# Kernel optimization log

Measured on AMD Instinct MI355X. Metric: run time of the kernel, lower is better.

The kernel has to match this reference:

```python
import jax, jax.numpy as jnp
import numpy as np

S, H, NH, DS = 4096, 1024, 2, 64   # seq_len, hidden, num_heads, static_in_size
HD = H // NH                        # head_dim = 512
EPS = 1e-5                          # eqx.nn.LayerNorm default eps


def setup_inputs() -> dict:
    key = jax.random.key(0)
    ks = jax.random.split(key, 11)
    sc = lambda n: 1.0 / np.sqrt(n)
    return {
        "inputs": jax.random.normal(ks[0], (S, H), jnp.float32),
        "static_data": jax.random.normal(ks[1], (DS,), jnp.float32),
        "base_mask": jax.random.randint(ks[2], (S,), 0, 2).astype(bool),
        "Wq": jax.random.normal(ks[3], (H, H), jnp.float32) * sc(H),
        "Wk": jax.random.normal(ks[4], (H, H), jnp.float32) * sc(H),
        "Wv": jax.random.normal(ks[5], (H, H), jnp.float32) * sc(H),
        "Wo": jax.random.normal(ks[6], (H, H), jnp.float32) * sc(H),
        "Ws": jax.random.normal(ks[7], (H, DS), jnp.float32) * sc(DS),
        "bs": jax.random.normal(ks[8], (H,), jnp.float32) * 0.01,
        "ln_w": jnp.ones((H,), jnp.float32),
        "ln_b": jnp.zeros((H,), jnp.float32),
    }


def reference(inputs, static_data, base_mask, Wq, Wk, Wv, Wo, Ws, bs, ln_w, ln_b):
    # static embedding injected into keys/values
    semb = Ws @ static_data + bs                      # [H]
    kv_in = inputs + semb[None, :]                    # [S, H]

    # per-head projections (eqx Linear: y = W @ x, no bias in MHA projections)
    q = (inputs @ Wq.T).reshape(S, NH, HD)
    k = (kv_in @ Wk.T).reshape(S, NH, HD)
    v = (kv_in @ Wv.T).reshape(S, NH, HD)

    logits = jnp.einsum('qhd,khd->hqk', q, k) / np.sqrt(HD)  # [NH, S, S]

    # head 0: irregular mask (base_mask broadcast over queries); head 1: all-ones
    irregular = jnp.broadcast_to(base_mask[None, :], (S, S))
    mask = jnp.stack([irregular, jnp.ones((S, S), bool)], axis=0)  # [2, S, S]
    logits = jnp.where(mask, logits, jnp.finfo(logits.dtype).min)

    attn = jax.nn.softmax(logits, axis=-1)
    ctx = jnp.einsum('hqk,khd->qhd', attn, v).reshape(S, H)
    out = ctx @ Wo.T                                  # output projection

    # dropout_rate = 0 -> identity; residual + per-token LayerNorm
    res = out + inputs
    mu = res.mean(-1, keepdims=True)
    var = res.var(-1, keepdims=True)
    return (res - mu) / jnp.sqrt(var + EPS) * ln_w + ln_b
```

## Files before the change

kernel.cpp:

```cpp
#include <hip/hip_runtime.h>
#include <stdint.h>

#define S_LEN  4096
#define HID    1024
#define NHEAD  2
#define HDIM   512
#define KS_STRIDE 520
#define LN_EPS 1e-5f
#define PADK   4224
#define CH1    832

typedef __bf16 bf16x8 __attribute__((ext_vector_type(8)));
typedef float  f32x4  __attribute__((ext_vector_type(4)));

__device__ __forceinline__ float b2f(unsigned short u) {
    return __uint_as_float(((unsigned int)u) << 16);
}
__device__ __forceinline__ unsigned short f2b(float f) {
    unsigned int u = __float_as_uint(f);
    u += 0x7FFFu + ((u >> 16) & 1u);
    return (unsigned short)(u >> 16);
}

__device__ __forceinline__ void async_cp16(const void* g, void* l) {
    __builtin_amdgcn_global_load_lds(
        (const __attribute__((address_space(1))) unsigned int*)g,
        (__attribute__((address_space(3))) unsigned int*)l, 16, 0, 0);
}

__global__ void k_cvt4s(const float* __restrict__ i0, const float* __restrict__ i1,
                        const float* __restrict__ i2, const float* __restrict__ i3,
                        unsigned short* __restrict__ o0, unsigned short* __restrict__ o1,
                        unsigned short* __restrict__ o2, unsigned short* __restrict__ o3,
                        const float* __restrict__ Ws, const float* __restrict__ sd,
                        const float* __restrict__ bs, float* __restrict__ semb,
                        const int* __restrict__ msk, int* __restrict__ cidx,
                        int* __restrict__ nactp) {
    int z = blockIdx.y;
    if (z == 4) {
        int j = blockIdx.x * blockDim.x + threadIdx.x;
        if (j >= HID) return;
        float acc = bs[j];
        const float* row = Ws + j * 64;
        #pragma unroll
        for (int d = 0; d < 64; ++d) acc += row[d] * sd[d];
        semb[j] = acc;
        return;
    }
    if (z == 5) {
        if (blockIdx.x != 0) return;
        __shared__ int cnts[256];
        __shared__ int bases[256];
        int t = threadIdx.x;
        int c = 0;
        #pragma unroll
        for (int i = 0; i < 16; ++i) c += (msk[t * 16 + i] != 0);
        cnts[t] = c;
        __syncthreads();
        if (t == 0) {
            int b = 0;
            for (int k = 0; k < 256; ++k) { bases[k] = b; b += cnts[k]; }
            nactp[0] = b;
        }
        __syncthreads();
        int b = bases[t];
        #pragma unroll
        for (int i = 0; i < 16; ++i)
            if (msk[t * 16 + i] != 0) cidx[b++] = t * 16 + i;
        return;
    }
    const float* in = z == 0 ? i0 : z == 1 ? i1 : z == 2 ? i2 : i3;
    unsigned short* o = z == 0 ? o0 : z == 1 ? o1 : z == 2 ? o2 : o3;
    int i = (blockIdx.x * blockDim.x + threadIdx.x) * 8;
    float4 a = *(const float4*)(in + i);
    float4 b = *(const float4*)(in + i + 4);
    unsigned short r[8] = {f2b(a.x), f2b(a.y), f2b(a.z), f2b(a.w),
                           f2b(b.x), f2b(b.y), f2b(b.z), f2b(b.w)};
    *(uint4*)(o + i) = *(const uint4*)r;
}

__global__ void k_kvin(const float* __restrict__ X,
                       const float* __restrict__ semb,
                       unsigned short* __restrict__ Xb,
                       unsigned short* __restrict__ kv) {
    int idx = (blockIdx.x * blockDim.x + threadIdx.x) * 8;
    if (idx >= S_LEN * HID) return;
    int col = idx & (HID - 1);
    float4 a = *(const float4*)(X + idx);
    float4 b = *(const float4*)(X + idx + 4);
    unsigned short xo[8] = {f2b(a.x), f2b(a.y), f2b(a.z), f2b(a.w),
                            f2b(b.x), f2b(b.y), f2b(b.z), f2b(b.w)};
    *(uint4*)(Xb + idx) = *(const uint4*)xo;
    unsigned short o[8];
    o[0] = f2b(a.x + semb[col + 0]);
    o[1] = f2b(a.y + semb[col + 1]);
    o[2] = f2b(a.z + semb[col + 2]);
    o[3] = f2b(a.w + semb[col + 3]);
    o[4] = f2b(b.x + semb[col + 4]);
    o[5] = f2b(b.y + semb[col + 5]);
    o[6] = f2b(b.z + semb[col + 6]);
    o[7] = f2b(b.w + semb[col + 7]);
    *(uint4*)(kv + idx) = *(const uint4*)o;
}

__device__ __forceinline__
void gemm128(const unsigned short* __restrict__ A,
             const unsigned short* __restrict__ B,
             unsigned short* __restrict__ Cb,
             int bx, int nx, int ldc) {
    __shared__ unsigned short As[2][128 * 32];
    __shared__ unsigned short Bs[2][128 * 32];
    int tid  = threadIdx.x;
    int wave = tid >> 6, lane = tid & 63;
    int quad = lane >> 4, l16 = lane & 15;
    int wm = wave >> 1, wn = wave & 1;
    int m0 = (bx / nx) * 128, n0 = (bx % nx) * 128;

    auto stage = [&](int k0, int b) {
        #pragma unroll
        for (int i = 0; i < 2; ++i) {
            int c = tid + i * 256;
            async_cp16(A + (m0 + (c >> 2)) * HID + k0 + (c & 3) * 8, As[b] + c * 8);
            async_cp16(B + (n0 + (c >> 2)) * HID + k0 + (c & 3) * 8, Bs[b] + c * 8);
        }
    };

    f32x4 zero = {0.f, 0.f, 0.f, 0.f};
    f32x4 acc[4][4];
    #pragma unroll
    for (int i = 0; i < 4; ++i)
        #pragma unroll
        for (int j = 0; j < 4; ++j) acc[i][j] = zero;

    stage(0, 0);
    for (int it = 0; it < HID / 32; ++it) {
        int b = it & 1;
        __syncthreads();
        if (it + 1 < HID / 32) stage((it + 1) * 32, b ^ 1);

        bf16x8 af[4], bfr[4];
        #pragma unroll
        for (int i = 0; i < 4; ++i)
            af[i] = *(const bf16x8*)(As[b] + (wm * 64 + i * 16 + l16) * 32 + quad * 8);
        #pragma unroll
        for (int j = 0; j < 4; ++j)
            bfr[j] = *(const bf16x8*)(Bs[b] + (wn * 64 + j * 16 + l16) * 32 + quad * 8);
        #pragma unroll
        for (int i = 0; i < 4; ++i)
            #pragma unroll
            for (int j = 0; j < 4; ++j)
                acc[i][j] = __builtin_amdgcn_mfma_f32_16x16x32_bf16(af[i], bfr[j], acc[i][j], 0, 0, 0);
    }

    #pragma unroll
    for (int i = 0; i < 4; ++i) {
        int rbase = m0 + wm * 64 + i * 16 + quad * 4;
        #pragma unroll
        for (int j = 0; j < 4; ++j) {
            int col = n0 + wn * 64 + j * 16 + l16;
            #pragma unroll
            for (int r = 0; r < 4; ++r)
                Cb[(size_t)(rbase + r) * ldc + col] = f2b(acc[i][j][r]);
        }
    }
}

__global__ __launch_bounds__(256)
void k_gemm_qkv(const unsigned short* __restrict__ Xb,
                const unsigned short* __restrict__ kvin,
                const unsigned short* __restrict__ Wqb,
                const unsigned short* __restrict__ Wkb,
                const unsigned short* __restrict__ Wvb,
                unsigned short* __restrict__ Qb,
                unsigned short* __restrict__ Kb,
                unsigned short* __restrict__ Vt) {
    int bx = (blockIdx.x & 7) * 32 + (blockIdx.x >> 3);
    int z = blockIdx.z;
    if (z == 0)      gemm128(Xb,   Wqb,  Qb,  bx,  8, HID);
    else if (z == 1) gemm128(kvin, Wkb,  Kb,  bx,  8, HID);
    else             gemm128(Wvb,  kvin, Vt,  bx, 32, S_LEN);
}

__global__ __launch_bounds__(256)
void k_gather(const unsigned short* __restrict__ Kb,
              const unsigned short* __restrict__ Vt,
              const int* __restrict__ cidx,
              const int* __restrict__ nactp,
              unsigned short* __restrict__ Kc,
              unsigned short* __restrict__ Vtc) {
    int nact = nactp[0];
    int gid = blockIdx.x * 256 + threadIdx.x;
    int idx = gid * 8;
    if (blockIdx.y == 0) {
        int j = idx >> 9, d = idx & 511;
        uint4 v = {0u, 0u, 0u, 0u};
        if (j < nact) v = *(const uint4*)(Kb + (size_t)cidx[j] * HID + d);
        *(uint4*)(Kc + (size_t)j * 512 + d) = v;
    } else {
        int d = idx / PADK, j0 = idx % PADK;
        unsigned short o[8];
        #pragma unroll
        for (int i = 0; i < 8; ++i) {
            int j = j0 + i;
            o[i] = (j < nact) ? Vt[(size_t)d * S_LEN + cidx[j]] : (unsigned short)0;
        }
        *(uint4*)(Vtc + (size_t)d * PADK + j0) = *(const uint4*)o;
    }
}

__global__ __launch_bounds__(256)
void k_gemm_o(const unsigned short* __restrict__ Opart,
              const float* __restrict__ Lbuf,
              const unsigned short* __restrict__ B,
              float* __restrict__ Cf,
              const float* __restrict__ Xres) {
    __shared__ unsigned short As[2][64 * 32];
    __shared__ unsigned short Bs[2][128 * 32];
    const size_t SH2 = (size_t)S_LEN * 512;
    int tid  = threadIdx.x;
    int wave = tid >> 6, lane = tid & 63;
    int quad = lane >> 4, l16 = lane & 15;
    int bx = (blockIdx.x & 7) * 64 + (blockIdx.x >> 3);
    int m0 = (bx >> 3) * 64, n0 = (bx & 7) * 128;

    int arow  = m0 + (tid >> 2);
    int acol8 = (tid & 3) * 8;
    float rinv[NHEAD];
    {
        float l0 = Lbuf[arow] + Lbuf[S_LEN + arow] + Lbuf[2 * S_LEN + arow];
        float l1 = 0.f;
        #pragma unroll
        for (int z = 3; z < 8; ++z) l1 += Lbuf[z * S_LEN + arow];
        rinv[0] = 1.f / l0;
        rinv[1] = 1.f / l1;
    }

    auto stageB = [&](int k0, int b) {
        #pragma unroll
        for (int i = 0; i < 2; ++i) {
            int c = tid + i * 256;
            async_cp16(B + (n0 + (c >> 2)) * HID + k0 + (c & 3) * 8, Bs[b] + c * 8);
        }
    };
    auto stageA = [&](int k0, int b) {
        int h = k0 >> 9;
        float rv = rinv[h];
        int lk = (k0 & 511) + acol8;
        const unsigned short* ap = Opart + (h ? 3 * SH2 : 0) + (size_t)arow * 512 + lk;
        float s[8] = {0.f, 0.f, 0.f, 0.f, 0.f, 0.f, 0.f, 0.f};
        int nz = h ? 5 : 3;
        for (int z = 0; z < nz; ++z) {
            uint4 v = *(const uint4*)(ap + (size_t)z * SH2);
            unsigned short us[8];
            *(uint4*)us = v;
            #pragma unroll
            for (int e = 0; e < 8; ++e) s[e] += b2f(us[e]);
        }
        unsigned short o8[8];
        #pragma unroll
        for (int e = 0; e < 8; ++e) o8[e] = f2b(s[e] * rv);
        *(uint4*)(As[b] + tid * 8) = *(const uint4*)o8;
    };

    f32x4 zero = {0.f, 0.f, 0.f, 0.f};
    f32x4 acc[4][2];
    #pragma unroll
    for (int i = 0; i < 4; ++i)
        #pragma unroll
        for (int j = 0; j < 2; ++j) acc[i][j] = zero;

    stageB(0, 0);
    stageA(0, 0);
    for (int it = 0; it < HID / 32; ++it) {
        int b = it & 1;
        __syncthreads();
        if (it + 1 < HID / 32) {
            stageB((it + 1) * 32, b ^ 1);
            stageA((it + 1) * 32, b ^ 1);
        }
        bf16x8 af[4], bfr[2];
        #pragma unroll
        for (int i = 0; i < 4; ++i)
            af[i] = *(const bf16x8*)(As[b] + (i * 16 + l16) * 32 + quad * 8);
        #pragma unroll
        for (int j = 0; j < 2; ++j)
            bfr[j] = *(const bf16x8*)(Bs[b] + (wave * 32 + j * 16 + l16) * 32 + quad * 8);
        #pragma unroll
        for (int i = 0; i < 4; ++i)
            #pragma unroll
            for (int j = 0; j < 2; ++j)
                acc[i][j] = __builtin_amdgcn_mfma_f32_16x16x32_bf16(af[i], bfr[j], acc[i][j], 0, 0, 0);
    }

    #pragma unroll
    for (int i = 0; i < 4; ++i) {
        int rbase = m0 + i * 16 + quad * 4;
        #pragma unroll
        for (int j = 0; j < 2; ++j) {
            int col = n0 + wave * 32 + j * 16 + l16;
            #pragma unroll
            for (int r = 0; r < 4; ++r) {
                size_t o = (size_t)(rbase + r) * HID + col;
                Cf[o] = acc[i][j][r] + Xres[o];
            }
        }
    }
}

__global__ __launch_bounds__(512, 2)
void k_flash(const unsigned short* __restrict__ Q,
             const unsigned short* __restrict__ Kb,
             const unsigned short* __restrict__ Vt,
             const unsigned short* __restrict__ Kc,
             const unsigned short* __restrict__ Vtc,
             const int* __restrict__ nactp,
             unsigned short* __restrict__ Opart,
             float* __restrict__ Lbuf) {
    __shared__ unsigned short Ks[2][32 * KS_STRIDE];
    __shared__ __bf16 Ps[2][128][40];
    int tid  = threadIdx.x;
    int wave = tid >> 6, lane = tid & 63;
    int quad = lane >> 4, l16 = lane & 15;
    int x = blockIdx.x, qtile = blockIdx.y;
    int head  = (x >= 3) ? 1 : 0;
    int split = head ? x - 3 : x;
    int nact  = nactp[0];

    int nit, base, krs, vrs;
    const unsigned short *Ksrc, *Vsrc;
    if (head == 0) {
        nit  = (nact + 95) / 96;
        base = split * nit * 32;
        Ksrc = Kc;  krs = 512;
        Vsrc = Vtc; vrs = PADK;
    } else {
        base = split * CH1;
        nit  = min(CH1 >> 5, (S_LEN - base) >> 5);
        Ksrc = Kb + HDIM;  krs = HID;
        Vsrc = Vt + (size_t)HDIM * S_LEN;
        vrs  = S_LEN;
    }

    int qrow = qtile * 128 + wave * 16 + l16;
    const unsigned short* qp = Q + qrow * HID + head * HDIM;
    bf16x8 qf[16];
    #pragma unroll
    for (int t = 0; t < 16; ++t) qf[t] = *(const bf16x8*)(qp + t * 32 + quad * 8);

    float lsum[4];
    #pragma unroll
    for (int r = 0; r < 4; ++r) lsum[r] = 0.f;
    f32x4 zero = {0.f, 0.f, 0.f, 0.f};
    f32x4 oacc[8][4];
    #pragma unroll
    for (int mt = 0; mt < 8; ++mt)
        #pragma unroll
        for (int nt = 0; nt < 4; ++nt) oacc[mt][nt] = zero;

    const float scale = 0.044194173824159216f;
    const unsigned short* vptr = Vsrc + (size_t)(wave * 64 + l16) * vrs + base + quad * 8;

    auto stageK = [&](int kt, int buf) {
        int kb = base + kt * 32;
        #pragma unroll
        for (int i = 0; i < 4; ++i) {
            int c = tid + i * 512;
            int row = c >> 6, col = (c & 63) * 8;
            async_cp16(Ksrc + (size_t)(kb + row) * krs + col, &Ks[buf][row * KS_STRIDE + col]);
        }
    };

    if (nit > 0) stageK(0, 0);

    bf16x8 vf[4];
    for (int it = 0; it < nit; ++it) {
        int cur = it & 1;
        __syncthreads();

        if (it + 1 < nit) stageK(it + 1, cur ^ 1);

        __builtin_amdgcn_s_setprio(1);
        if (it > 0) {
            #pragma unroll
            for (int mt = 0; mt < 8; ++mt) {
                bf16x8 pf = *(const bf16x8*)&Ps[cur ^ 1][mt * 16 + l16][quad * 8];
                #pragma unroll
                for (int nt = 0; nt < 4; ++nt)
                    oacc[mt][nt] = __builtin_amdgcn_mfma_f32_16x16x32_bf16(pf, vf[nt], oacc[mt][nt], 0, 0, 0);
            }
        }

        #pragma unroll
        for (int nt = 0; nt < 4; ++nt)
            vf[nt] = *(const bf16x8*)(vptr + (size_t)nt * 16 * vrs + it * 32);

        f32x4 sacc[2];
        sacc[0] = zero; sacc[1] = zero;
        #pragma unroll
        for (int nt = 0; nt < 2; ++nt)
            #pragma unroll
            for (int t = 0; t < 16; ++t) {
                bf16x8 kf = *(const bf16x8*)&Ks[cur][(nt * 16 + l16) * KS_STRIDE + t * 32 + quad * 8];
                sacc[nt] = __builtin_amdgcn_mfma_f32_16x16x32_bf16(qf[t], kf, sacc[nt], 0, 0, 0);
            }
        __builtin_amdgcn_s_setprio(0);

        bool keep0 = true, keep1 = true;
        if (head == 0) {
            int kb = base + it * 32;
            keep0 = kb + l16 < nact;
            keep1 = kb + 16 + l16 < nact;
        }
        #pragma unroll
        for (int r = 0; r < 4; ++r) {
            float p0 = keep0 ? __expf(fminf(sacc[0][r] * scale, 30.f)) : 0.f;
            float p1 = keep1 ? __expf(fminf(sacc[1][r] * scale, 30.f)) : 0.f;
            lsum[r] += p0 + p1;
            Ps[cur][wave * 16 + quad * 4 + r][l16]      = (__bf16)p0;
            Ps[cur][wave * 16 + quad * 4 + r][16 + l16] = (__bf16)p1;
        }
    }

    if (nit > 0) {
        int lastb = (nit - 1) & 1;
        __syncthreads();
        #pragma unroll
        for (int mt = 0; mt < 8; ++mt) {
            bf16x8 pf = *(const bf16x8*)&Ps[lastb][mt * 16 + l16][quad * 8];
            #pragma unroll
            for (int nt = 0; nt < 4; ++nt)
                oacc[mt][nt] = __builtin_amdgcn_mfma_f32_16x16x32_bf16(pf, vf[nt], oacc[mt][nt], 0, 0, 0);
        }
    }

    #pragma unroll
    for (int r = 0; r < 4; ++r) {
        float s = lsum[r];
        #pragma unroll
        for (int off = 1; off < 16; off <<= 1)
            s += __shfl_xor(s, off, 64);
        lsum[r] = s;
    }
    int slot = head ? 3 + split : split;
    int lrow = qtile * 128 + wave * 16 + quad * 4;
    if (l16 == 0) {
        #pragma unroll
        for (int r = 0; r < 4; ++r)
            Lbuf[slot * S_LEN + lrow + r] = lsum[r];
    }
    unsigned short* op = Opart + (size_t)slot * S_LEN * 512;
    #pragma unroll
    for (int mt = 0; mt < 8; ++mt)
        #pragma unroll
        for (int nt = 0; nt < 4; ++nt)
            #pragma unroll
            for (int r = 0; r < 4; ++r)
                op[(qtile * 128 + mt * 16 + quad * 4 + r) * 512 +
                   wave * 64 + nt * 16 + l16] = f2b(oacc[mt][nt][r]);
}

__global__ __launch_bounds__(256)
void k_ln(const float* __restrict__ res,
          const float* __restrict__ w,
          const float* __restrict__ b,
          float* __restrict__ out) {
    __shared__ float red[8];
    int s = blockIdx.x, tid = threadIdx.x;
    const float* row = res + s * HID;
    float x[4], s1 = 0.f, s2 = 0.f;
    #pragma unroll
    for (int i = 0; i < 4; ++i) {
        x[i] = row[tid + i * 256];
        s1 += x[i]; s2 += x[i] * x[i];
    }
    #pragma unroll
    for (int off = 1; off < 64; off <<= 1) {
        s1 += __shfl_xor(s1, off, 64);
        s2 += __shfl_xor(s2, off, 64);
    }
    int wave = tid >> 6;
    if ((tid & 63) == 0) { red[wave] = s1; red[4 + wave] = s2; }
    __syncthreads();
    s1 = red[0] + red[1] + red[2] + red[3];
    s2 = red[4] + red[5] + red[6] + red[7];
    float mu   = s1 * (1.f / HID);
    float var  = s2 * (1.f / HID) - mu * mu;
    float rstd = rsqrtf(var + LN_EPS);
    #pragma unroll
    for (int i = 0; i < 4; ++i) {
        int col = tid + i * 256;
        out[s * HID + col] = (x[i] - mu) * rstd * w[col] + b[col];
    }
}

extern "C" void kernel_launch(void* const* d_in, const int* in_sizes, int n_in,
                              void* d_out, int out_size, void* d_ws, size_t ws_size,
                              hipStream_t stream) {
    const float* X   = (const float*)d_in[0];
    const float* sd  = (const float*)d_in[1];
    const int*   msk = (const int*)d_in[2];
    const float* Wq  = (const float*)d_in[3];
    const float* Wk  = (const float*)d_in[4];
    const float* Wv  = (const float*)d_in[5];
    const float* Wo  = (const float*)d_in[6];
    const float* Wsp = (const float*)d_in[7];
    const float* bsp = (const float*)d_in[8];
    const float* lw  = (const float*)d_in[9];
    const float* lb  = (const float*)d_in[10];
    float* out = (float*)d_out;

    char* ws = (char*)d_ws;
    const size_t MB = 1ull << 20;
    float*          semb  = (float*)(ws);
    int*            cidx  = (int*)(ws + (16 << 10));
    int*            nactp = (int*)(ws + (48 << 10));
    float*          Lbuf  = (float*)(ws + (1ull << 16));
    unsigned short* Xb    = (unsigned short*)(ws + 1 * MB);
    unsigned short* kvin  = (unsigned short*)(ws + 9 * MB);
    unsigned short* Kc    = (unsigned short*)(ws + 1 * MB);
    unsigned short* Vtc   = (unsigned short*)(ws + 5 * MB + (256 << 10));
    unsigned short* Qb    = (unsigned short*)(ws + 17 * MB);
    unsigned short* Kb    = (unsigned short*)(ws + 25 * MB);
    unsigned short* Vt    = (unsigned short*)(ws + 33 * MB);
    unsigned short* Wqb   = (unsigned short*)(ws + 49 * MB);
    unsigned short* Wkb   = (unsigned short*)(ws + 51 * MB);
    unsigned short* Wvb   = (unsigned short*)(ws + 53 * MB);
    unsigned short* Wob   = (unsigned short*)(ws + 55 * MB);
    float*          resf  = (float*)(ws + 17 * MB);
    unsigned short* Opart = (unsigned short*)(ws + 57 * MB);

    const int SH = S_LEN * HID;
    const int WW = HID * HID;

    k_cvt4s<<<dim3(WW / 8 / 256, 6), dim3(256), 0, stream>>>(
        Wq, Wk, Wv, Wo, Wqb, Wkb, Wvb, Wob, Wsp, sd, bsp, semb, msk, cidx, nactp);

    k_kvin<<<dim3(SH / 8 / 256), dim3(256), 0, stream>>>(X, semb, Xb, kvin);

    k_gemm_qkv<<<dim3(256, 1, 3), dim3(256), 0, stream>>>(Xb, kvin, Wqb, Wkb, Wvb, Qb, Kb, Vt);

    k_gather<<<dim3(PADK * 512 / 8 / 256, 2), dim3(256), 0, stream>>>(
        Kb, Vt, cidx, nactp, Kc, Vtc);

    k_flash<<<dim3(8, S_LEN / 128), dim3(512), 0, stream>>>(
        Qb, Kb, Vt, Kc, Vtc, nactp, Opart, Lbuf);

    k_gemm_o<<<dim3(512), dim3(256), 0, stream>>>(Opart, Lbuf, Wob, resf, X);
    k_ln<<<dim3(S_LEN), dim3(256), 0, stream>>>(resf, lw, lb, out);
}
```

Before: 270.3 us.

## Fuse masked-key gather into the QKV projection GEMM via indexed row loads

Removes the separate gather kernel. The projection GEMM now computes head-0 K and V directly into compacted buffers, using the active-index list to choose which input rows it loads, and computes head-1 K/V into dedicated half-width buffers. Padded index entries are zero-filled so tiles past the active count read row 0 rather than garbage. This removes a kernel launch and the gather's read/write traffic, and skips projecting masked head-0 keys, but adds an indirect index load per staged row and a less uniform block dispatch.

```diff
diff --git a/kernel.cpp b/kernel.cpp
--- a/kernel.cpp
+++ b/kernel.cpp
@@ -51,6 +51,7 @@
         if (blockIdx.x != 0) return;
         __shared__ int cnts[256];
         __shared__ int bases[256];
+        __shared__ int nact_s;
         int t = threadIdx.x;
         int c = 0;
         #pragma unroll
@@ -61,12 +62,14 @@
             int b = 0;
             for (int k = 0; k < 256; ++k) { bases[k] = b; b += cnts[k]; }
             nactp[0] = b;
+            nact_s   = b;
         }
         __syncthreads();
         int b = bases[t];
         #pragma unroll
         for (int i = 0; i < 16; ++i)
             if (msk[t * 16 + i] != 0) cidx[b++] = t * 16 + i;
+        for (int j = nact_s + t; j < PADK; j += 256) cidx[j] = 0;
         return;
     }
     const float* in = z == 0 ? i0 : z == 1 ? i1 : z == 2 ? i2 : i3;
@@ -107,7 +110,8 @@
 void gemm128(const unsigned short* __restrict__ A,
              const unsigned short* __restrict__ B,
              unsigned short* __restrict__ Cb,
-             int bx, int nx, int ldc) {
+             int bx, int nx, int ldc,
+             const int* __restrict__ ra, const int* __restrict__ rb) {
     __shared__ unsigned short As[2][128 * 32];
     __shared__ unsigned short Bs[2][128 * 32];
     int tid  = threadIdx.x;
@@ -120,8 +124,12 @@
         #pragma unroll
         for (int i = 0; i < 2; ++i) {
             int c = tid + i * 256;
-            async_cp16(A + (m0 + (c >> 2)) * HID + k0 + (c & 3) * 8, As[b] + c * 8);
-            async_cp16(B + (n0 + (c >> 2)) * HID + k0 + (c & 3) * 8, Bs[b] + c * 8);
+            int arow = m0 + (c >> 2);
+            if (ra) arow = ra[arow];
+            int brow = n0 + (c >> 2);
+            if (rb) brow = rb[brow];
+            async_cp16(A + (size_t)arow * HID + k0 + (c & 3) * 8, As[b] + c * 8);
+            async_cp16(B + (size_t)brow * HID + k0 + (c & 3) * 8, Bs[b] + c * 8);
         }
     };
 
@@ -166,46 +174,24 @@
 }
 
 __global__ __launch_bounds__(256)
-void k_gemm_qkv(const unsigned short* __restrict__ Xb,
-                const unsigned short* __restrict__ kvin,
-                const unsigned short* __restrict__ Wqb,
-                const unsigned short* __restrict__ Wkb,
-                const unsigned short* __restrict__ Wvb,
-                unsigned short* __restrict__ Qb,
-                unsigned short* __restrict__ Kb,
-                unsigned short* __restrict__ Vt) {
-    int bx = (blockIdx.x & 7) * 32 + (blockIdx.x >> 3);
-    int z = blockIdx.z;
-    if (z == 0)      gemm128(Xb,   Wqb,  Qb,  bx,  8, HID);
-    else if (z == 1) gemm128(kvin, Wkb,  Kb,  bx,  8, HID);
-    else             gemm128(Wvb,  kvin, Vt,  bx, 32, S_LEN);
-}
-
-__global__ __launch_bounds__(256)
-void k_gather(const unsigned short* __restrict__ Kb,
-              const unsigned short* __restrict__ Vt,
-              const int* __restrict__ cidx,
-              const int* __restrict__ nactp,
-              unsigned short* __restrict__ Kc,
-              unsigned short* __restrict__ Vtc) {
-    int nact = nactp[0];
-    int gid = blockIdx.x * 256 + threadIdx.x;
-    int idx = gid * 8;
-    if (blockIdx.y == 0) {
-        int j = idx >> 9, d = idx & 511;
-        uint4 v = {0u, 0u, 0u, 0u};
-        if (j < nact) v = *(const uint4*)(Kb + (size_t)cidx[j] * HID + d);
-        *(uint4*)(Kc + (size_t)j * 512 + d) = v;
-    } else {
-        int d = idx / PADK, j0 = idx % PADK;
-        unsigned short o[8];
-        #pragma unroll
-        for (int i = 0; i < 8; ++i) {
-            int j = j0 + i;
-            o[i] = (j < nact) ? Vt[(size_t)d * S_LEN + cidx[j]] : (unsigned short)0;
-        }
-        *(uint4*)(Vtc + (size_t)d * PADK + j0) = *(const uint4*)o;
-    }
+void k_gemms(const unsigned short* __restrict__ Xb,
+             const unsigned short* __restrict__ kvin,
+             const unsigned short* __restrict__ Wqb,
+             const unsigned short* __restrict__ Wkb,
+             const unsigned short* __restrict__ Wvb,
+             const int* __restrict__ cidx,
+             unsigned short* __restrict__ Qb,
+             unsigned short* __restrict__ Kb1,
+             unsigned short* __restrict__ Vt1,
+             unsigned short* __restrict__ Kc,
+             unsigned short* __restrict__ Vtc) {
+    int g = blockIdx.x;
+    int b = (g & 7) * 97 + (g >> 3);
+    if (b < 256)      gemm128(Xb,   Wqb,             Qb,  b,        8, HID,   nullptr, nullptr);
+    else if (b < 384) gemm128(kvin, Wkb + 512 * HID, Kb1, b - 256,  4, 512,   nullptr, nullptr);
+    else if (b < 512) gemm128(Wvb + 512 * HID, kvin, Vt1, b - 384, 32, S_LEN, nullptr, nullptr);
+    else if (b < 644) gemm128(kvin, Wkb,             Kc,  b - 512,  4, 512,   cidx,    nullptr);
+    else              gemm128(Wvb,  kvin,            Vtc, b - 644, 33, PADK,  nullptr, cidx);
 }
 
 __global__ __launch_bounds__(256)
@@ -309,8 +295,8 @@
 
 __global__ __launch_bounds__(512, 2)
 void k_flash(const unsigned short* __restrict__ Q,
-             const unsigned short* __restrict__ Kb,
-             const unsigned short* __restrict__ Vt,
+             const unsigned short* __restrict__ Kb1,
+             const unsigned short* __restrict__ Vt1,
              const unsigned short* __restrict__ Kc,
              const unsigned short* __restrict__ Vtc,
              const int* __restrict__ nactp,
@@ -326,19 +312,16 @@
     int split = head ? x - 3 : x;
     int nact  = nactp[0];
 
-    int nit, base, krs, vrs;
+    int nit, base, vrs;
     const unsigned short *Ksrc, *Vsrc;
     if (head == 0) {
         nit  = (nact + 95) / 96;
         base = split * nit * 32;
-        Ksrc = Kc;  krs = 512;
-        Vsrc = Vtc; vrs = PADK;
+        Ksrc = Kc;  Vsrc = Vtc; vrs = PADK;
     } else {
         base = split * CH1;
         nit  = min(CH1 >> 5, (S_LEN - base) >> 5);
-        Ksrc = Kb + HDIM;  krs = HID;
-        Vsrc = Vt + (size_t)HDIM * S_LEN;
-        vrs  = S_LEN;
+        Ksrc = Kb1; Vsrc = Vt1; vrs = S_LEN;
     }
 
     int qrow = qtile * 128 + wave * 16 + l16;
@@ -366,7 +349,7 @@
         for (int i = 0; i < 4; ++i) {
             int c = tid + i * 512;
             int row = c >> 6, col = (c & 63) * 8;
-            async_cp16(Ksrc + (size_t)(kb + row) * krs + col, &Ks[buf][row * KS_STRIDE + col]);
+            async_cp16(Ksrc + (size_t)(kb + row) * 512 + col, &Ks[buf][row * KS_STRIDE + col]);
         }
     };
 
@@ -517,11 +500,11 @@
     float*          Lbuf  = (float*)(ws + (1ull << 16));
     unsigned short* Xb    = (unsigned short*)(ws + 1 * MB);
     unsigned short* kvin  = (unsigned short*)(ws + 9 * MB);
-    unsigned short* Kc    = (unsigned short*)(ws + 1 * MB);
-    unsigned short* Vtc   = (unsigned short*)(ws + 5 * MB + (256 << 10));
     unsigned short* Qb    = (unsigned short*)(ws + 17 * MB);
-    unsigned short* Kb    = (unsigned short*)(ws + 25 * MB);
-    unsigned short* Vt    = (unsigned short*)(ws + 33 * MB);
+    unsigned short* Kb1   = (unsigned short*)(ws + 25 * MB);
+    unsigned short* Vt1   = (unsigned short*)(ws + 29 * MB);
+    unsigned short* Kc    = (unsigned short*)(ws + 33 * MB);
+    unsigned short* Vtc   = (unsigned short*)(ws + 37 * MB + (256 << 10));
     unsigned short* Wqb   = (unsigned short*)(ws + 49 * MB);
     unsigned short* Wkb   = (unsigned short*)(ws + 51 * MB);
     unsigned short* Wvb   = (unsigned short*)(ws + 53 * MB);
@@ -537,13 +520,11 @@
 
     k_kvin<<<dim3(SH / 8 / 256), dim3(256), 0, stream>>>(X, semb, Xb, kvin);
 
-    k_gemm_qkv<<<dim3(256, 1, 3), dim3(256), 0, stream>>>(Xb, kvin, Wqb, Wkb, Wvb, Qb, Kb, Vt);
-
-    k_gather<<<dim3(PADK * 512 / 8 / 256, 2), dim3(256), 0, stream>>>(
-        Kb, Vt, cidx, nactp, Kc, Vtc);
+    k_gemms<<<dim3(776), dim3(256), 0, stream>>>(
+        Xb, kvin, Wqb, Wkb, Wvb, cidx, Qb, Kb1, Vt1, Kc, Vtc);
 
     k_flash<<<dim3(8, S_LEN / 128), dim3(512), 0, stream>>>(
-        Qb, Kb, Vt, Kc, Vtc, nactp, Opart, Lbuf);
+        Qb, Kb1, Vt1, Kc, Vtc, nactp, Opart, Lbuf);
 
     k_gemm_o<<<dim3(512), dim3(256), 0, stream>>>(Opart, Lbuf, Wob, resf, X);
     k_ln<<<dim3(S_LEN), dim3(256), 0, stream>>>(resf, lw, lb, out);
```

After: 269.0 us. No clear change (-0.5%).
